# Kernel optimization log

Hardware: AMD Instinct MI355X
Metric: run time of the kernel (lower is better)

The kernel has to match this reference:

```python
import jax, jax.numpy as jnp
import numpy as np

HEADS = 16
KV_HEADS = 4
DIM_HEAD = 64
DIM = 1024
B, N = 2, 2048


def setup_inputs() -> dict:
    key = jax.random.key(0)
    k1, k2, k3 = jax.random.split(key, 3)
    x = jax.random.normal(k1, (B, N, DIM), dtype=jnp.float32)
    Wq = jax.random.normal(k2, (DIM, HEADS * DIM_HEAD), dtype=jnp.float32) / np.sqrt(DIM)
    Wkv = jax.random.normal(k3, (DIM, 2 * KV_HEADS * DIM_HEAD), dtype=jnp.float32) / np.sqrt(DIM)
    k_scale = jnp.ones((HEADS, 1, DIM_HEAD), dtype=jnp.float32)
    return {"x": x, "Wq": Wq, "Wkv": Wkv, "k_scale": k_scale}


def reference(x, Wq, Wkv, k_scale):
    b, n, _ = x.shape
    g = HEADS // KV_HEADS  # query heads per kv head
    scale = DIM_HEAD ** -0.5
    # fused qkv projections (no bias)
    q = (x @ Wq).reshape(b, n, HEADS, DIM_HEAD)
    kv = x @ Wkv
    k, v = jnp.split(kv, 2, axis=-1)
    k = k.reshape(b, n, KV_HEADS, DIM_HEAD).transpose(0, 2, 1, 3)  # b k n d
    v = v.reshape(b, n, KV_HEADS, DIM_HEAD).transpose(0, 2, 1, 3)  # b k n d
    # group query heads: b, kv_heads, g, n, d
    qg = q.transpose(0, 2, 1, 3).reshape(b, KV_HEADS, g, n, DIM_HEAD)
    # per-query-head k scale, applied to the group-broadcast k (qk-norm)
    ks = k_scale.reshape(KV_HEADS, g, 1, DIM_HEAD)
    kk = k[:, :, None, :, :] * ks  # b k g n d
    dots = jnp.einsum('bkgid,bkgjd->bkgij', qg, kk) * scale
    attn = jax.nn.softmax(dots, axis=-1)
    out = jnp.einsum('bkgij,bkjd->bkgid', attn, v)  # v broadcast over g
    out = out.reshape(b, HEADS, n, DIM_HEAD).transpose(0, 2, 1, 3).reshape(b, n, HEADS * DIM_HEAD)
    return out
```

## Files before the change

kernel.cpp:

```cpp
#include <hip/hip_runtime.h>
#include <stdint.h>
#include <math.h>

typedef __attribute__((ext_vector_type(8))) __bf16 bf16x8;
typedef __attribute__((ext_vector_type(4))) float f32x4;
typedef __attribute__((ext_vector_type(16))) float f32x16;

__device__ __forceinline__ uint32_t f32_to_bf16_rne(float f) {
  union { float f; uint32_t u; } v; v.f = f;
  return (v.u + 0x7FFFu + ((v.u >> 16) & 1u)) >> 16;
}

__device__ __forceinline__ uint32_t cvt_pk_bf16(float lo, float hi) {
  uint32_t r;
  asm("v_cvt_pk_bf16_f32 %0, %1, %2" : "=v"(r) : "v"(lo), "v"(hi));
  return r;
}

__device__ __forceinline__ void gld16(void* lds, const void* g) {
  __builtin_amdgcn_global_load_lds(
      (__attribute__((address_space(1))) void*)(g),
      (__attribute__((address_space(3))) void*)(lds), 16, 0, 0);
}

__device__ __forceinline__ f32x4 mfma16(bf16x8 a, bf16x8 b, f32x4 c) {
  return __builtin_amdgcn_mfma_f32_16x16x32_bf16(a, b, c, 0, 0, 0);
}
__device__ __forceinline__ f32x16 mfma32(bf16x8 a, bf16x8 b, f32x16 c) {
  return __builtin_amdgcn_mfma_f32_32x32x16_bf16(a, b, c, 0, 0, 0);
}

#define LOG2E 1.44269504088896340736f

__global__ __launch_bounds__(256) void k_convert(const float* __restrict__ x,
                                                 const float* __restrict__ wq,
                                                 const float* __restrict__ wkv,
                                                 uint16_t* __restrict__ xb,
                                                 uint16_t* __restrict__ wt) {
  __shared__ float tile[64][65];
  int blk = blockIdx.x;
  int t = threadIdx.x;
  if (blk < 2048) {
    int i = blk * 256 + t;
    const float4* xv = (const float4*)x;
    float4 a = xv[2 * i], b2 = xv[2 * i + 1];
    uint32_t w0 = f32_to_bf16_rne(a.x) | (f32_to_bf16_rne(a.y) << 16);
    uint32_t w1 = f32_to_bf16_rne(a.z) | (f32_to_bf16_rne(a.w) << 16);
    uint32_t w2 = f32_to_bf16_rne(b2.x) | (f32_to_bf16_rne(b2.y) << 16);
    uint32_t w3 = f32_to_bf16_rne(b2.z) | (f32_to_bf16_rne(b2.w) << 16);
    ((uint4*)xb)[i] = make_uint4(w0, w1, w2, w3);
  } else {
    int blk2 = blk - 2048;
    int c0 = (blk2 % 24) * 64, k0 = (blk2 / 24) * 64;
    int col = t & 63, rq = t >> 6;
#pragma unroll
    for (int rr = 0; rr < 16; rr++) {
      int r = rr * 4 + rq;
      int c = c0 + col;
      float v = (c < 1024) ? wq[(uint64_t)(k0 + r) * 1024 + c]
                           : wkv[(uint64_t)(k0 + r) * 512 + (c - 1024)];
      tile[r][col] = v;
    }
    __syncthreads();
#pragma unroll
    for (int rr = 0; rr < 16; rr++) {
      int a = rr * 4 + rq;
      wt[(uint64_t)(c0 + a) * 1024 + k0 + col] = (uint16_t)f32_to_bf16_rne(tile[col][a]);
    }
  }
}

__global__ __launch_bounds__(256, 2) void k_proj_gemm(
    const uint16_t* __restrict__ xb, const uint16_t* __restrict__ wt,
    const float* __restrict__ kscale, uint16_t* __restrict__ q_ws,
    uint16_t* __restrict__ kf_ws, uint16_t* __restrict__ vf_ws) {
  __shared__ __align__(16) uint16_t ring[3][12288];
  int t = threadIdx.x;
  int w = t >> 6, l = t & 63;
  int lq = l & 15, lg = l >> 4;
  int m0 = blockIdx.x * 128, n0 = blockIdx.y * 64;
  int wr = w >> 1, wc = w & 1;
  f32x4 acc[4][2] = {};

  auto stage = [&](int slot, int k0) {
#pragma unroll
    for (int j = 0; j < 4; j++) {
      int c = j * 256 + t;
      int r = c >> 3, s = c & 7;
      int sl = s ^ (r & 7);
      gld16((char*)&ring[slot][0] + c * 16,
            xb + (uint64_t)(m0 + r) * 1024 + k0 + sl * 8);
    }
#pragma unroll
    for (int j = 0; j < 2; j++) {
      int c = j * 256 + t;
      int r = c >> 3, s = c & 7;
      int sl = s ^ (r & 7);
      gld16((char*)&ring[slot][8192] + c * 16,
            wt + (uint64_t)(n0 + r) * 1024 + k0 + sl * 8);
    }
  };

  stage(0, 0);
  stage(1, 64);
  asm volatile("s_waitcnt vmcnt(6)" ::: "memory");
  __builtin_amdgcn_s_barrier();

  for (int it = 0; it < 16; ++it) {
    int tn = it + 2;
    int kn = (tn < 16) ? tn * 64 : (tn - 3) * 64;
    stage(tn % 3, kn);
    asm volatile("s_waitcnt vmcnt(6)" ::: "memory");
    __builtin_amdgcn_s_barrier();

    const uint16_t* As = &ring[it % 3][0];
    const uint16_t* Bs = &ring[it % 3][8192];
    bf16x8 af[2][4], bfr[2][2];
#pragma unroll
    for (int kk = 0; kk < 2; kk++) {
#pragma unroll
      for (int m = 0; m < 4; m++) {
        int r = wr * 64 + m * 16 + lq;
        int sl = (kk * 4 + lg) ^ (r & 7);
        af[kk][m] = *(const bf16x8*)(As + r * 64 + sl * 8);
      }
#pragma unroll
      for (int n = 0; n < 2; n++) {
        int r = wc * 32 + n * 16 + lq;
        int sl = (kk * 4 + lg) ^ (r & 7);
        bfr[kk][n] = *(const bf16x8*)(Bs + r * 64 + sl * 8);
      }
    }
    __builtin_amdgcn_s_setprio(1);
#pragma unroll
    for (int kk = 0; kk < 2; kk++)
#pragma unroll
      for (int m = 0; m < 4; m++)
#pragma unroll
        for (int n = 0; n < 2; n++)
          acc[m][n] = mfma16(af[kk][m], bfr[kk][n], acc[m][n]);
    __builtin_amdgcn_s_setprio(0);
  }

#pragma unroll
  for (int m = 0; m < 4; m++)
#pragma unroll
    for (int n = 0; n < 2; n++)
#pragma unroll
      for (int jj = 0; jj < 4; jj++) {
        int row = m0 + wr * 64 + m * 16 + 4 * lg + jj;
        int col = n0 + wc * 32 + n * 16 + lq;
        float val = acc[m][n][jj];
        int b = row >> 11, nn = row & 2047;
        if (col < 1024) {
          val *= kscale[col] * 0.125f * LOG2E;
          q_ws[((uint64_t)((b * 16 + (col >> 6)) * 2048 + nn)) * 64 + (col & 63)] =
              (uint16_t)f32_to_bf16_rne(val);
        } else if (col < 1280) {
          int kvh = (col - 1024) >> 6;
          int d = col & 63;
          int gsu = nn >> 5, lrr = nn & 31;
          int mm = d >> 4, hh = (d >> 3) & 1, el = d & 7;
          kf_ws[(uint64_t)(b * 4 + kvh) * 131072 +
                (uint64_t)((((gsu * 4 + mm) * 64) + hh * 32 + lrr) * 8 + el)] =
              (uint16_t)f32_to_bf16_rne(val);
        } else {
          int kvh = (col - 1280) >> 6;
          int d = col & 63;
          int gsu = nn >> 5, jj2 = (nn >> 4) & 1, hh = (nn >> 3) & 1, el = nn & 7;
          int dd = d >> 5, lrr = d & 31;
          vf_ws[(uint64_t)(b * 4 + kvh) * 131072 +
                (uint64_t)((((gsu * 4 + dd * 2 + jj2) * 64) + hh * 32 + lrr) * 8 + el)] =
              (uint16_t)f32_to_bf16_rne(val);
        }
      }
}

__global__ __launch_bounds__(512, 1) void k_attn(const uint16_t* __restrict__ q_ws,
                                                 const uint16_t* __restrict__ kf_ws,
                                                 const uint16_t* __restrict__ vf_ws,
                                                 float* __restrict__ out) {
  extern __shared__ __align__(16) char smem[];

  int t = threadIdx.x, w = t >> 6, l = t & 63;
  int lr = l & 31, hi = l >> 5;
  int qg = w & 3, half = w >> 2;
  int blk = blockIdx.x;
  int c = blk & 7, j = blk >> 3;
  int b = c >> 2, kvh = c & 3;
  int h = kvh * 4 + (j >> 3), qb = j & 7;

  const uint16_t* Qb = q_ws + (uint64_t)(b * 16 + h) * 2048 * 64;
  const uint16_t* Kh = kf_ws + (uint64_t)(b * 4 + kvh) * 131072 + (uint64_t)half * 65536;
  const uint16_t* Vh = vf_ws + (uint64_t)(b * 4 + kvh) * 131072 + (uint64_t)half * 65536;
  int qrow0 = qb * 256 + qg * 64;

  bf16x8 qfA[4], qfB[4];
#pragma unroll
  for (int m = 0; m < 4; m++) {
    qfA[m] = *(const bf16x8*)(Qb + (uint64_t)(qrow0 + lr) * 64 + m * 16 + hi * 8);
    qfB[m] = *(const bf16x8*)(Qb + (uint64_t)(qrow0 + 32 + lr) * 64 + m * 16 + hi * 8);
  }

  f32x16 oaccA[2] = {}, oaccB[2] = {};
  float lA = 0.f, lB = 0.f;

  char* myLDS = smem + w * 16384;

  auto stage = [&](int slot, int sul) {
    char* d = myLDS + slot * 8192 + l * 16;
    const uint16_t* ks = Kh + (uint64_t)sul * 2048 + l * 8;
    const uint16_t* vs = Vh + (uint64_t)sul * 2048 + l * 8;
#pragma unroll
    for (int f = 0; f < 4; f++) gld16(d + f * 1024, ks + f * 512);
#pragma unroll
    for (int f = 0; f < 4; f++) gld16(d + 4096 + f * 1024, vs + f * 512);
  };

  auto qk = [&](const bf16x8* kf, const bf16x8* qf) {
    f32x16 T = {};
    __builtin_amdgcn_s_setprio(1);
#pragma unroll
    for (int m = 0; m < 4; m++) T = mfma32(kf[m], qf[m], T);
    __builtin_amdgcn_s_setprio(0);
    return T;
  };

  auto finish = [&](f32x16& Tc, const bf16x8* vf, f32x16* oacc, float& lsum) {
    float p[16];
#pragma unroll
    for (int e = 0; e < 16; e++) p[e] = __builtin_amdgcn_exp2f(Tc[e]);
    float sm0 = ((p[0] + p[1]) + (p[2] + p[3])) + ((p[4] + p[5]) + (p[6] + p[7]));
    float sm1 = ((p[8] + p[9]) + (p[10] + p[11])) + ((p[12] + p[13]) + (p[14] + p[15]));
    lsum += sm0 + sm1;

    bf16x8 pa[2];
#pragma unroll
    for (int jj = 0; jj < 2; jj++) {
      const float* pp = p + 8 * jj;
      uint32_t X = cvt_pk_bf16(pp[0], pp[1]);
      uint32_t Z = cvt_pk_bf16(pp[2], pp[3]);
      uint32_t Y = cvt_pk_bf16(pp[4], pp[5]);
      uint32_t W2 = cvt_pk_bf16(pp[6], pp[7]);
      asm volatile("v_permlane32_swap_b32 %0, %1" : "+v"(X), "+v"(Y));
      asm volatile("v_permlane32_swap_b32 %0, %1" : "+v"(Z), "+v"(W2));
      union { uint32_t u[4]; bf16x8 v; } pu;
      pu.u[0] = X; pu.u[1] = Z; pu.u[2] = Y; pu.u[3] = W2;
      pa[jj] = pu.v;
    }

    __builtin_amdgcn_s_setprio(1);
#pragma unroll
    for (int dd = 0; dd < 2; dd++)
#pragma unroll
      for (int jj = 0; jj < 2; jj++)
        oacc[dd] = mfma32(pa[jj], vf[dd * 2 + jj], oacc[dd]);
    __builtin_amdgcn_s_setprio(0);
  };

  stage(0, 0);

  for (int su = 0; su < 32; ++su) {
    int sn = (su + 1 > 31) ? 31 : su + 1;
    stage((su + 1) & 1, sn);
    asm volatile("s_waitcnt vmcnt(8)" ::: "memory");

    const uint16_t* base = (const uint16_t*)(myLDS + (su & 1) * 8192);
    bf16x8 kf[4];
#pragma unroll
    for (int m = 0; m < 4; m++) kf[m] = *(const bf16x8*)(base + m * 512 + l * 8);
    f32x16 Ta = qk(kf, qfA);
    f32x16 Tb = qk(kf, qfB);
    bf16x8 vf[4];
#pragma unroll
    for (int i = 0; i < 4; i++) vf[i] = *(const bf16x8*)(base + (4 + i) * 512 + l * 8);
    finish(Ta, vf, oaccA, lA);
    finish(Tb, vf, oaccB, lB);
  }

  lA += __shfl_xor(lA, 32);
  lB += __shfl_xor(lB, 32);

  asm volatile("s_waitcnt vmcnt(0)" ::: "memory");
  __syncthreads();

  float* exch = (float*)smem;
  float* exl = (float*)(smem + 65536);
  if (half == 1) {
#pragma unroll
    for (int sub = 0; sub < 2; sub++) {
      f32x16* oacc = sub ? oaccB : oaccA;
#pragma unroll
      for (int r = 0; r < 16; r++) {
        int qr = (r & 3) + 8 * (r >> 2) + 4 * hi;
        exch[qg * 4096 + (sub * 32 + qr) * 64 + lr] = oacc[0][r];
        exch[qg * 4096 + (sub * 32 + qr) * 64 + 32 + lr] = oacc[1][r];
      }
    }
    if (hi == 0) {
      exl[qg * 64 + lr] = lA;
      exl[qg * 64 + 32 + lr] = lB;
    }
  }
  __syncthreads();
  if (half == 0) {
    lA += exl[qg * 64 + lr];
    lB += exl[qg * 64 + 32 + lr];
    float invA = 1.0f / lA, invB = 1.0f / lB;
#pragma unroll
    for (int sub = 0; sub < 2; sub++) {
      f32x16* oacc = sub ? oaccB : oaccA;
      float inv = sub ? invB : invA;
#pragma unroll
      for (int r = 0; r < 16; r++) {
        int qr = (r & 3) + 8 * (r >> 2) + 4 * hi;
        float iv = __shfl(inv, qr);
        float o0 = oacc[0][r] + exch[qg * 4096 + (sub * 32 + qr) * 64 + lr];
        float o1 = oacc[1][r] + exch[qg * 4096 + (sub * 32 + qr) * 64 + 32 + lr];
        float* orow =
            out + (uint64_t)(b * 2048 + qrow0 + sub * 32 + qr) * 1024 + h * 64 + lr;
        orow[0] = o0 * iv;
        orow[32] = o1 * iv;
      }
    }
  }
}

extern "C" void kernel_launch(void* const* d_in, const int* in_sizes, int n_in,
                              void* d_out, int out_size, void* d_ws, size_t ws_size,
                              hipStream_t stream) {
  const float* x = (const float*)d_in[0];
  const float* wq = (const float*)d_in[1];
  const float* wkv = (const float*)d_in[2];
  const float* kscale = (const float*)d_in[3];
  float* out = (float*)d_out;
  char* ws = (char*)d_ws;
  uint16_t* xb = (uint16_t*)(ws);
  uint16_t* wt = (uint16_t*)(ws + (8ull << 20));
  uint16_t* q_ws = (uint16_t*)(ws + (11ull << 20));
  uint16_t* kf_ws = (uint16_t*)(ws + (19ull << 20));
  uint16_t* vf_ws = (uint16_t*)(ws + (21ull << 20));

  static bool attr_set = false;
  if (!attr_set) {
    (void)hipFuncSetAttribute((const void*)k_attn,
                              hipFuncAttributeMaxDynamicSharedMemorySize, 131072);
    attr_set = true;
  }

  k_convert<<<2432, 256, 0, stream>>>(x, wq, wkv, xb, wt);
  k_proj_gemm<<<dim3(32, 24), 256, 0, stream>>>(xb, wt, kscale, q_ws, kf_ws, vf_ws);
  k_attn<<<256, 512, 131072, stream>>>(q_ws, kf_ws, vf_ws, out);
}
```

Before: 80.82 us.

## Share K/V staging across waves, shrink attention blocks, remap GEMM tiles per XCD

The attention kernel drops from 8 to 4 waves per block with 128 query rows. Each pair of waves now cooperatively loads K and V into a shared 4-slot LDS ring, where before each wave kept its own private double-buffered copy. This halves LDS use so four blocks can share a CU, and it deepens prefetch to three stages at the cost of a block-wide barrier every iteration. The projection GEMM launches a 1D grid remapped so that row tiles are grouped by XCD for L2 reuse, and its wait and barrier move to the end of each iteration.

```diff
diff --git a/kernel.cpp b/kernel.cpp
--- a/kernel.cpp
+++ b/kernel.cpp
@@ -78,7 +78,10 @@
   int t = threadIdx.x;
   int w = t >> 6, l = t & 63;
   int lq = l & 15, lg = l >> 4;
-  int m0 = blockIdx.x * 128, n0 = blockIdx.y * 64;
+  int id = blockIdx.x;
+  int xcd = id & 7, idx = id >> 3;
+  int rrp = idx & 3, cc = idx >> 2;
+  int m0 = (xcd * 4 + rrp) * 128, n0 = cc * 64;
   int wr = w >> 1, wc = w & 1;
   f32x4 acc[4][2] = {};
 
@@ -110,8 +113,6 @@
     int tn = it + 2;
     int kn = (tn < 16) ? tn * 64 : (tn - 3) * 64;
     stage(tn % 3, kn);
-    asm volatile("s_waitcnt vmcnt(6)" ::: "memory");
-    __builtin_amdgcn_s_barrier();
 
     const uint16_t* As = &ring[it % 3][0];
     const uint16_t* Bs = &ring[it % 3][8192];
@@ -140,6 +141,9 @@
         for (int n = 0; n < 2; n++)
           acc[m][n] = mfma16(af[kk][m], bfr[kk][n], acc[m][n]);
     __builtin_amdgcn_s_setprio(0);
+
+    asm volatile("s_waitcnt vmcnt(6) lgkmcnt(0)" ::: "memory");
+    __builtin_amdgcn_s_barrier();
   }
 
 #pragma unroll
@@ -176,7 +180,7 @@
       }
 }
 
-__global__ __launch_bounds__(512, 1) void k_attn(const uint16_t* __restrict__ q_ws,
+__global__ __launch_bounds__(256, 4) void k_attn(const uint16_t* __restrict__ q_ws,
                                                  const uint16_t* __restrict__ kf_ws,
                                                  const uint16_t* __restrict__ vf_ws,
                                                  float* __restrict__ out) {
@@ -184,16 +188,16 @@
 
   int t = threadIdx.x, w = t >> 6, l = t & 63;
   int lr = l & 31, hi = l >> 5;
-  int qg = w & 3, half = w >> 2;
+  int qg = w & 1, half = w >> 1;
   int blk = blockIdx.x;
   int c = blk & 7, j = blk >> 3;
   int b = c >> 2, kvh = c & 3;
-  int h = kvh * 4 + (j >> 3), qb = j & 7;
+  int h = kvh * 4 + (j >> 4), qb = j & 15;
 
   const uint16_t* Qb = q_ws + (uint64_t)(b * 16 + h) * 2048 * 64;
-  const uint16_t* Kh = kf_ws + (uint64_t)(b * 4 + kvh) * 131072 + (uint64_t)half * 65536;
-  const uint16_t* Vh = vf_ws + (uint64_t)(b * 4 + kvh) * 131072 + (uint64_t)half * 65536;
-  int qrow0 = qb * 256 + qg * 64;
+  const uint16_t* Kb = kf_ws + (uint64_t)(b * 4 + kvh) * 131072;
+  const uint16_t* Vb = vf_ws + (uint64_t)(b * 4 + kvh) * 131072;
+  int qrow0 = qb * 128 + qg * 64;
 
   bf16x8 qfA[4], qfB[4];
 #pragma unroll
@@ -205,16 +209,17 @@
   f32x16 oaccA[2] = {}, oaccB[2] = {};
   float lA = 0.f, lB = 0.f;
 
-  char* myLDS = smem + w * 16384;
+  const uint16_t* SbW = (qg ? Vb : Kb) + (uint64_t)half * 65536 + l * 8;
+  char* dstW = smem + half * 8192 + qg * 4096 + l * 16;
 
   auto stage = [&](int slot, int sul) {
-    char* d = myLDS + slot * 8192 + l * 16;
-    const uint16_t* ks = Kh + (uint64_t)sul * 2048 + l * 8;
-    const uint16_t* vs = Vh + (uint64_t)sul * 2048 + l * 8;
-#pragma unroll
-    for (int f = 0; f < 4; f++) gld16(d + f * 1024, ks + f * 512);
-#pragma unroll
-    for (int f = 0; f < 4; f++) gld16(d + 4096 + f * 1024, vs + f * 512);
+    char* d = dstW + slot * 16384;
+    const uint16_t* s = SbW + (uint64_t)sul * 2048;
+#pragma unroll
+    for (int f = 0; f < 4; f++) gld16(d + f * 1024, s + f * 512);
+  };
+  auto slotbase = [&](int slot) {
+    return (const uint16_t*)(smem + slot * 16384 + half * 8192);
   };
 
   auto qk = [&](const bf16x8* kf, const bf16x8* qf) {
@@ -259,13 +264,17 @@
   };
 
   stage(0, 0);
+  stage(1, 1);
+  stage(2, 2);
+  asm volatile("s_waitcnt vmcnt(8)" ::: "memory");
+  __builtin_amdgcn_s_barrier();
 
   for (int su = 0; su < 32; ++su) {
-    int sn = (su + 1 > 31) ? 31 : su + 1;
-    stage((su + 1) & 1, sn);
-    asm volatile("s_waitcnt vmcnt(8)" ::: "memory");
-
-    const uint16_t* base = (const uint16_t*)(myLDS + (su & 1) * 8192);
+    int sn = su + 3;
+    if (sn > 31) sn = 31;
+    stage((su + 3) & 3, sn);
+
+    const uint16_t* base = slotbase(su & 3);
     bf16x8 kf[4];
 #pragma unroll
     for (int m = 0; m < 4; m++) kf[m] = *(const bf16x8*)(base + m * 512 + l * 8);
@@ -276,6 +285,9 @@
     for (int i = 0; i < 4; i++) vf[i] = *(const bf16x8*)(base + (4 + i) * 512 + l * 8);
     finish(Ta, vf, oaccA, lA);
     finish(Tb, vf, oaccB, lB);
+
+    asm volatile("s_waitcnt vmcnt(8) lgkmcnt(0)" ::: "memory");
+    __builtin_amdgcn_s_barrier();
   }
 
   lA += __shfl_xor(lA, 32);
@@ -285,7 +297,7 @@
   __syncthreads();
 
   float* exch = (float*)smem;
-  float* exl = (float*)(smem + 65536);
+  float* exl = (float*)(smem + 32768);
   if (half == 1) {
 #pragma unroll
     for (int sub = 0; sub < 2; sub++) {
@@ -344,11 +356,11 @@
   static bool attr_set = false;
   if (!attr_set) {
     (void)hipFuncSetAttribute((const void*)k_attn,
-                              hipFuncAttributeMaxDynamicSharedMemorySize, 131072);
+                              hipFuncAttributeMaxDynamicSharedMemorySize, 65536);
     attr_set = true;
   }
 
   k_convert<<<2432, 256, 0, stream>>>(x, wq, wkv, xb, wt);
-  k_proj_gemm<<<dim3(32, 24), 256, 0, stream>>>(xb, wt, kscale, q_ws, kf_ws, vf_ws);
-  k_attn<<<256, 512, 131072, stream>>>(q_ws, kf_ws, vf_ws, out);
-}
+  k_proj_gemm<<<768, 256, 0, stream>>>(xb, wt, kscale, q_ws, kf_ws, vf_ws);
+  k_attn<<<512, 256, 65536, stream>>>(q_ws, kf_ws, vf_ws, out);
+}
```

Result: slower. 173.7 us (+114.9%).
